# Optimization experiments

Hardware: AMD Instinct MI355X
Metric: run time of the kernel (lower is better)

Reference implementation:

```python
import jax, jax.numpy as jnp
import numpy as np

N = 50000      # nodes
E = 400000     # edges (before self-loops)
F_IN = 128     # input_embedding_dim
HID = 256      # hidden_dim
HEADS = 4      # gat_heads
C1 = HID // HEADS  # per-head channels layer 0
OUT = 128      # output_node_dim
G = 64         # graphs in batch
NEG_SLOPE = 0.2


def setup_inputs() -> dict:
    key = jax.random.key(0)
    ks = jax.random.split(key, 12)
    s = lambda fan: 1.0 / np.sqrt(fan)
    embedded_x = jax.random.normal(ks[0], (N, F_IN), jnp.float32)
    edge_index = jax.random.randint(ks[1], (2, E), 0, N, dtype=jnp.int32)
    batch_idx = jnp.sort(jax.random.randint(ks[2], (N,), 0, G, dtype=jnp.int32))
    # layer 0: GATConv(F_IN -> C1, heads=HEADS, concat=True)
    W1 = jax.random.normal(ks[3], (F_IN, HEADS * C1), jnp.float32) * s(F_IN)
    att_src1 = jax.random.normal(ks[4], (HEADS, C1), jnp.float32) * s(C1)
    att_dst1 = jax.random.normal(ks[5], (HEADS, C1), jnp.float32) * s(C1)
    b1 = jnp.zeros((HEADS * C1,), jnp.float32)
    # layer 1 (last): GATConv(HID -> OUT, heads=1, concat=False)
    W2 = jax.random.normal(ks[6], (HID, OUT), jnp.float32) * s(HID)
    att_src2 = jax.random.normal(ks[7], (1, OUT), jnp.float32) * s(OUT)
    att_dst2 = jax.random.normal(ks[8], (1, OUT), jnp.float32) * s(OUT)
    b2 = jnp.zeros((OUT,), jnp.float32)
    return {"embedded_x": embedded_x, "edge_index": edge_index, "batch_idx": batch_idx,
            "W1": W1, "att_src1": att_src1, "att_dst1": att_dst1, "b1": b1,
            "W2": W2, "att_src2": att_src2, "att_dst2": att_dst2, "b2": b2}


def gat_conv(x, src, dst, W, att_src, att_dst, bias, heads, out_ch, concat):
    n = x.shape[0]
    xw = (x @ W).reshape(n, heads, out_ch)              # [N,H,C]
    a_s = (xw * att_src[None]).sum(-1)                  # [N,H]
    a_d = (xw * att_dst[None]).sum(-1)                  # [N,H]
    e = jax.nn.leaky_relu(a_s[src] + a_d[dst], NEG_SLOPE)  # [E',H]
    # segment softmax over incoming edges of each dst node (self-loops guarantee non-empty)
    m = jax.ops.segment_max(e, dst, num_segments=n)
    ee = jnp.exp(e - m[dst])
    denom = jax.ops.segment_sum(ee, dst, num_segments=n)
    alpha = ee / denom[dst]                             # [E',H]
    msg = xw[src] * alpha[:, :, None]                   # [E',H,C]
    out = jax.ops.segment_sum(msg, dst, num_segments=n) # [N,H,C]
    out = out.reshape(n, heads * out_ch) if concat else out.mean(axis=1)
    return out + bias


def reference(embedded_x, edge_index, batch_idx, W1, att_src1, att_dst1, b1, W2, att_src2, att_dst2, b2):
    loops = jnp.arange(N, dtype=edge_index.dtype)
    src = jnp.concatenate([edge_index[0], loops])
    dst = jnp.concatenate([edge_index[1], loops])
    h = gat_conv(embedded_x, src, dst, W1, att_src1, att_dst1, b1, HEADS, C1, True)
    h = jax.nn.elu(h)  # dropout is identity in eval
    h = gat_conv(h, src, dst, W2, att_src2, att_dst2, b2, 1, OUT, False)
    h = jax.nn.elu(h)
    # final_node_transform is Identity (current_dim == output_node_dim)
    counts = jax.ops.segment_sum(jnp.ones((N,), h.dtype), batch_idx, num_segments=G)
    graph_embedding = jax.ops.segment_sum(h, batch_idx, num_segments=G) / jnp.maximum(counts, 1.0)[:, None]
    return (graph_embedding, h)
```

## Files before the change

### kernel.cpp

```cpp
#include <hip/hip_runtime.h>

#define NN   50000
#define NE   400000
#define NET  450000
#define NG   64
#define NEG  0.2f

using bf16x8 = __attribute__((ext_vector_type(8))) short;
using f32x4  = __attribute__((ext_vector_type(4))) float;

__device__ inline float b2f(unsigned short u){
  union{unsigned int i; float f;} v; v.i = ((unsigned int)u) << 16; return v.f;
}
__device__ inline unsigned short f2b(float f){
  union{float f; unsigned int i;} v; v.f = f;
  unsigned int r = (v.i + 0x7fffu + ((v.i >> 16) & 1u)) >> 16;
  return (unsigned short)r;
}
__device__ inline float sane(float o){
  return (o > -1e30f && o < 1e30f) ? o : 0.f;
}
__device__ inline float lrelu_clamp(float e){
  e = e > 0.f ? e : NEG * e;
  return fminf(e, 60.f);
}

__global__ void pack_w(const float* __restrict__ W, unsigned short* __restrict__ Bp,
                       int K, int N){
  int t = blockIdx.x * blockDim.x + threadIdx.x;
  int nk = K / 32;
  int total = (N / 16) * nk * 64;
  if (t >= total) return;
  int lane = t & 63; int rest = t >> 6;
  int kit = rest % nk; int nt = rest / nk;
  int quad = lane >> 4, n = lane & 15;
  unsigned short* dst = Bp + (size_t)t * 8;
#pragma unroll
  for (int j = 0; j < 8; j++)
    dst[j] = f2b(W[(size_t)(kit*32 + quad*8 + j) * N + nt*16 + n]);
}

__global__ void gemm1_fused(const float* __restrict__ X, const unsigned short* __restrict__ Bp,
                            const float* __restrict__ av, const float* __restrict__ dv,
                            unsigned short* __restrict__ C,
                            float* __restrict__ a_s, float* __restrict__ a_d){
  constexpr int NK = 4, NT = 16;
  int lane = threadIdx.x & 63, wave = threadIdx.x >> 6;
  int mbase = (blockIdx.x * 4 + wave) * 16;
  if (mbase >= NN) return;
  int quad = lane >> 4, nn = lane & 15;
  int arow = mbase + nn; if (arow >= NN) arow = NN - 1;
  const float* Xr = X + (size_t)arow * 128 + quad * 8;
  bf16x8 afrag[NK];
#pragma unroll
  for (int kit = 0; kit < NK; kit++){
    bf16x8 a;
#pragma unroll
    for (int j = 0; j < 8; j++) a[j] = (short)f2b(Xr[kit * 32 + j]);
    afrag[kit] = a;
  }
  float sd0=0,sd1=0,sd2=0,sd3=0, dd0=0,dd1=0,dd2=0,dd3=0;
#pragma unroll
  for (int nt = 0; nt < NT; nt++){
    f32x4 acc = {0.f, 0.f, 0.f, 0.f};
#pragma unroll
    for (int kit = 0; kit < NK; kit++){
      bf16x8 bfrag = *(const bf16x8*)(Bp + ((size_t)(nt*NK + kit) * 64 + lane) * 8);
      acc = __builtin_amdgcn_mfma_f32_16x16x32_bf16(afrag[kit], bfrag, acc, 0, 0, 0);
    }
    int col = nt * 16 + nn;
    float avc = av[col], dvc = dv[col];
    sd0 += acc[0]*avc; dd0 += acc[0]*dvc;
    sd1 += acc[1]*avc; dd1 += acc[1]*dvc;
    sd2 += acc[2]*avc; dd2 += acc[2]*dvc;
    sd3 += acc[3]*avc; dd3 += acc[3]*dvc;
#pragma unroll
    for (int r = 0; r < 4; r++){
      int row = mbase + quad * 4 + r;
      if (row < NN) C[(size_t)row * 256 + col] = f2b(acc[r]);
    }
    if ((nt & 3) == 3){
      int hh = nt >> 2;
#pragma unroll
      for (int off = 1; off < 16; off <<= 1){
        sd0 += __shfl_xor(sd0, off); sd1 += __shfl_xor(sd1, off);
        sd2 += __shfl_xor(sd2, off); sd3 += __shfl_xor(sd3, off);
        dd0 += __shfl_xor(dd0, off); dd1 += __shfl_xor(dd1, off);
        dd2 += __shfl_xor(dd2, off); dd3 += __shfl_xor(dd3, off);
      }
      if (nn == 0){
        int row = mbase + quad * 4;
        if (row + 0 < NN){ a_s[(row+0)*4+hh] = sd0; a_d[(row+0)*4+hh] = dd0; }
        if (row + 1 < NN){ a_s[(row+1)*4+hh] = sd1; a_d[(row+1)*4+hh] = dd1; }
        if (row + 2 < NN){ a_s[(row+2)*4+hh] = sd2; a_d[(row+2)*4+hh] = dd2; }
        if (row + 3 < NN){ a_s[(row+3)*4+hh] = sd3; a_d[(row+3)*4+hh] = dd3; }
      }
      sd0=sd1=sd2=sd3=dd0=dd1=dd2=dd3=0.f;
    }
  }
}

__global__ void gemm2_fused(const unsigned short* __restrict__ A, const unsigned short* __restrict__ Bp,
                            const float* __restrict__ av, const float* __restrict__ dv,
                            unsigned short* __restrict__ C,
                            float* __restrict__ a_s, float* __restrict__ a_d){
  constexpr int NK = 8, NT = 8;
  int lane = threadIdx.x & 63, wave = threadIdx.x >> 6;
  int mbase = (blockIdx.x * 4 + wave) * 16;
  if (mbase >= NN) return;
  int quad = lane >> 4, nn = lane & 15;
  int arow = mbase + nn; if (arow >= NN) arow = NN - 1;
  const unsigned short* Ar = A + (size_t)arow * 256 + quad * 8;
  bf16x8 afrag[NK];
#pragma unroll
  for (int kit = 0; kit < NK; kit++)
    afrag[kit] = *(const bf16x8*)(Ar + kit * 32);
  float sd0=0,sd1=0,sd2=0,sd3=0, dd0=0,dd1=0,dd2=0,dd3=0;
#pragma unroll
  for (int nt = 0; nt < NT; nt++){
    f32x4 acc = {0.f, 0.f, 0.f, 0.f};
#pragma unroll
    for (int kit = 0; kit < NK; kit++){
      bf16x8 bfrag = *(const bf16x8*)(Bp + ((size_t)(nt*NK + kit) * 64 + lane) * 8);
      acc = __builtin_amdgcn_mfma_f32_16x16x32_bf16(afrag[kit], bfrag, acc, 0, 0, 0);
    }
    int col = nt * 16 + nn;
    float avc = av[col], dvc = dv[col];
    sd0 += acc[0]*avc; dd0 += acc[0]*dvc;
    sd1 += acc[1]*avc; dd1 += acc[1]*dvc;
    sd2 += acc[2]*avc; dd2 += acc[2]*dvc;
    sd3 += acc[3]*avc; dd3 += acc[3]*dvc;
#pragma unroll
    for (int r = 0; r < 4; r++){
      int row = mbase + quad * 4 + r;
      if (row < NN) C[(size_t)row * 128 + col] = f2b(acc[r]);
    }
  }
#pragma unroll
  for (int off = 1; off < 16; off <<= 1){
    sd0 += __shfl_xor(sd0, off); sd1 += __shfl_xor(sd1, off);
    sd2 += __shfl_xor(sd2, off); sd3 += __shfl_xor(sd3, off);
    dd0 += __shfl_xor(dd0, off); dd1 += __shfl_xor(dd1, off);
    dd2 += __shfl_xor(dd2, off); dd3 += __shfl_xor(dd3, off);
  }
  if (nn == 0){
    int row = mbase + quad * 4;
    if (row + 0 < NN){ a_s[row+0] = sd0; a_d[row+0] = dd0; }
    if (row + 1 < NN){ a_s[row+1] = sd1; a_d[row+1] = dd1; }
    if (row + 2 < NN){ a_s[row+2] = sd2; a_d[row+2] = dd2; }
    if (row + 3 < NN){ a_s[row+3] = sd3; a_d[row+3] = dd3; }
  }
}

__global__ void count_deg(const int* __restrict__ ei, int* __restrict__ deg){
  int t = blockIdx.x * blockDim.x + threadIdx.x;
  if (t >= NET) return;
  int d = (t < NE) ? ei[NE + t] : (t - NE);
  if (d < 0) d = 0; if (d >= NN) d = NN - 1;
  atomicAdd(&deg[d], 1);
}

__global__ void scan_block(const int* __restrict__ in, int* __restrict__ out_excl,
                           int* __restrict__ bsums, int n){
  __shared__ int s[256];
  int tid = threadIdx.x, gid = blockIdx.x * 256 + tid;
  int v = (gid < n) ? in[gid] : 0;
  s[tid] = v; __syncthreads();
  for (int off = 1; off < 256; off <<= 1){
    int t = (tid >= off) ? s[tid - off] : 0;
    __syncthreads();
    s[tid] += t;
    __syncthreads();
  }
  if (gid < n) out_excl[gid] = s[tid] - v;
  if (tid == 255) bsums[blockIdx.x] = s[255];
}

__global__ void scan_sums(int* __restrict__ bs, int nb){
  __shared__ int s[256];
  int tid = threadIdx.x;
  int v = (tid < nb) ? bs[tid] : 0;
  s[tid] = v; __syncthreads();
  for (int off = 1; off < 256; off <<= 1){
    int t = (tid >= off) ? s[tid - off] : 0;
    __syncthreads();
    s[tid] += t;
    __syncthreads();
  }
  if (tid < nb) bs[tid] = s[tid] - v;
}

__global__ void scan_add(int* __restrict__ offs, const int* __restrict__ bs,
                         int* __restrict__ cursor, int n){
  int gid = blockIdx.x * 256 + threadIdx.x;
  if (gid < n){
    int o = offs[gid] + bs[blockIdx.x];
    offs[gid] = o; cursor[gid] = o;
  }
  if (gid == 0) offs[n] = NET;
}

__global__ void fill_csr(const int* __restrict__ ei, int* __restrict__ cursor,
                         int* __restrict__ csr){
  int t = blockIdx.x * blockDim.x + threadIdx.x;
  if (t >= NET) return;
  int s = (t < NE) ? ei[t]      : (t - NE);
  int d = (t < NE) ? ei[NE + t] : (t - NE);
  if (d < 0) d = 0; if (d >= NN) d = NN - 1;
  int pos = atomicAdd(&cursor[d], 1);
  if (pos >= 0 && pos < NET) csr[pos] = s;
}

__global__ void agg1(const unsigned short* __restrict__ xw, const float* __restrict__ a_s,
                     const float* __restrict__ a_d, const int* __restrict__ offs,
                     const int* __restrict__ csr, const float* __restrict__ bias,
                     unsigned short* __restrict__ h1){
  int lane = threadIdx.x & 63;
  int node = (blockIdx.x * blockDim.x + threadIdx.x) >> 6;
  if (node >= NN) return;
  int h = lane >> 4;
  int beg = offs[node], end = offs[node + 1];
  if (beg < 0) beg = 0; if (end > NET) end = NET;
  float adv = a_d[node * 4 + h];
  float l0=0,l1=0,l2=0,l3=0;
  float c00=0,c01=0,c02=0,c03=0;
  float c10=0,c11=0,c12=0,c13=0;
  float c20=0,c21=0,c22=0,c23=0;
  float c30=0,c31=0,c32=0,c33=0;
  int e = beg;
  for (; e + 4 <= end; e += 4){
    int s0 = csr[e], s1 = csr[e+1], s2 = csr[e+2], s3 = csr[e+3];
    float p0 = __expf(lrelu_clamp(a_s[s0*4+h] + adv));
    float p1 = __expf(lrelu_clamp(a_s[s1*4+h] + adv));
    float p2 = __expf(lrelu_clamp(a_s[s2*4+h] + adv));
    float p3 = __expf(lrelu_clamp(a_s[s3*4+h] + adv));
    ushort4 x0 = *(const ushort4*)(xw + (size_t)s0 * 256 + lane * 4);
    ushort4 x1 = *(const ushort4*)(xw + (size_t)s1 * 256 + lane * 4);
    ushort4 x2 = *(const ushort4*)(xw + (size_t)s2 * 256 + lane * 4);
    ushort4 x3 = *(const ushort4*)(xw + (size_t)s3 * 256 + lane * 4);
    l0 += p0; c00 += p0*b2f(x0.x); c01 += p0*b2f(x0.y); c02 += p0*b2f(x0.z); c03 += p0*b2f(x0.w);
    l1 += p1; c10 += p1*b2f(x1.x); c11 += p1*b2f(x1.y); c12 += p1*b2f(x1.z); c13 += p1*b2f(x1.w);
    l2 += p2; c20 += p2*b2f(x2.x); c21 += p2*b2f(x2.y); c22 += p2*b2f(x2.z); c23 += p2*b2f(x2.w);
    l3 += p3; c30 += p3*b2f(x3.x); c31 += p3*b2f(x3.y); c32 += p3*b2f(x3.z); c33 += p3*b2f(x3.w);
  }
  for (; e < end; e++){
    int s0 = csr[e];
    float p0 = __expf(lrelu_clamp(a_s[s0*4+h] + adv));
    ushort4 x0 = *(const ushort4*)(xw + (size_t)s0 * 256 + lane * 4);
    l0 += p0; c00 += p0*b2f(x0.x); c01 += p0*b2f(x0.y); c02 += p0*b2f(x0.z); c03 += p0*b2f(x0.w);
  }
  float l = l0 + l1 + l2 + l3;
  float C0 = c00 + c10 + c20 + c30;
  float C1 = c01 + c11 + c21 + c31;
  float C2 = c02 + c12 + c22 + c32;
  float C3 = c03 + c13 + c23 + c33;
  if (!(l > 0.f)) l = 1.f;
  float inv = 1.f / l;
  float4 b4 = *(const float4*)(bias + lane * 4);
  float v; ushort4 o;
  v = C0 * inv + b4.x; v = v > 0.f ? v : expm1f(v); o.x = f2b(sane(v));
  v = C1 * inv + b4.y; v = v > 0.f ? v : expm1f(v); o.y = f2b(sane(v));
  v = C2 * inv + b4.z; v = v > 0.f ? v : expm1f(v); o.z = f2b(sane(v));
  v = C3 * inv + b4.w; v = v > 0.f ? v : expm1f(v); o.w = f2b(sane(v));
  *(ushort4*)(h1 + (size_t)node * 256 + lane * 4) = o;
}

__global__ void agg2(const unsigned short* __restrict__ xw, const float* __restrict__ a_s,
                     const float* __restrict__ a_d, const int* __restrict__ offs,
                     const int* __restrict__ csr, const float* __restrict__ bias,
                     float* __restrict__ hout){
  int lane = threadIdx.x & 63;
  int node = (blockIdx.x * blockDim.x + threadIdx.x) >> 6;
  if (node >= NN) return;
  int beg = offs[node], end = offs[node + 1];
  if (beg < 0) beg = 0; if (end > NET) end = NET;
  float adv = a_d[node];
  float l0=0,l1=0,l2=0,l3=0;
  float c00=0,c01=0, c10=0,c11=0, c20=0,c21=0, c30=0,c31=0;
  int e = beg;
  for (; e + 4 <= end; e += 4){
    int s0 = csr[e], s1 = csr[e+1], s2 = csr[e+2], s3 = csr[e+3];
    float p0 = __expf(lrelu_clamp(a_s[s0] + adv));
    float p1 = __expf(lrelu_clamp(a_s[s1] + adv));
    float p2 = __expf(lrelu_clamp(a_s[s2] + adv));
    float p3 = __expf(lrelu_clamp(a_s[s3] + adv));
    ushort2 x0 = *(const ushort2*)(xw + (size_t)s0 * 128 + lane * 2);
    ushort2 x1 = *(const ushort2*)(xw + (size_t)s1 * 128 + lane * 2);
    ushort2 x2 = *(const ushort2*)(xw + (size_t)s2 * 128 + lane * 2);
    ushort2 x3 = *(const ushort2*)(xw + (size_t)s3 * 128 + lane * 2);
    l0 += p0; c00 += p0*b2f(x0.x); c01 += p0*b2f(x0.y);
    l1 += p1; c10 += p1*b2f(x1.x); c11 += p1*b2f(x1.y);
    l2 += p2; c20 += p2*b2f(x2.x); c21 += p2*b2f(x2.y);
    l3 += p3; c30 += p3*b2f(x3.x); c31 += p3*b2f(x3.y);
  }
  for (; e < end; e++){
    int s0 = csr[e];
    float p0 = __expf(lrelu_clamp(a_s[s0] + adv));
    ushort2 x0 = *(const ushort2*)(xw + (size_t)s0 * 128 + lane * 2);
    l0 += p0; c00 += p0*b2f(x0.x); c01 += p0*b2f(x0.y);
  }
  float l = l0 + l1 + l2 + l3;
  float C0 = c00 + c10 + c20 + c30;
  float C1 = c01 + c11 + c21 + c31;
  if (!(l > 0.f)) l = 1.f;
  float inv = 1.f / l;
  float v0 = C0 * inv + bias[lane*2];   v0 = v0 > 0.f ? v0 : expm1f(v0);
  float v1 = C1 * inv + bias[lane*2+1]; v1 = v1 > 0.f ? v1 : expm1f(v1);
  float2 o; o.x = sane(v0); o.y = sane(v1);
  *(float2*)(hout + (size_t)node * 128 + lane * 2) = o;
}

__global__ void pool_kernel(const float* __restrict__ h, const int* __restrict__ batch,
                            float* __restrict__ pools, int* __restrict__ cnt){
  int c = threadIdx.x;
  int n0 = blockIdx.x * 64;
  if (n0 >= NN) return;
  int nend = n0 + 64; if (nend > NN) nend = NN;
  int cur = batch[n0];
  cur = (cur < 0) ? 0 : (cur >= NG ? NG - 1 : cur);
  float sum = 0.f; int count = 0;
  for (int n = n0; n < nend; n++){
    int g = batch[n];
    g = (g < 0) ? 0 : (g >= NG ? NG - 1 : g);
    if (g != cur){
      atomicAdd(&pools[cur * 128 + c], sum);
      if (c == 0) atomicAdd(&cnt[cur], count);
      sum = 0.f; count = 0; cur = g;
    }
    sum += h[(size_t)n * 128 + c];
    count++;
  }
  atomicAdd(&pools[cur * 128 + c], sum);
  if (c == 0) atomicAdd(&cnt[cur], count);
}

__global__ void final_kernel(const float* __restrict__ pools, const int* __restrict__ cnt,
                             float* __restrict__ out){
  int g = blockIdx.x, c = threadIdx.x;
  float d = fmaxf((float)cnt[g], 1.0f);
  out[g * 128 + c] = sane(pools[g * 128 + c] / d);
}

extern "C" void kernel_launch(void* const* d_in, const int* in_sizes, int n_in,
                              void* d_out, int out_size, void* d_ws, size_t ws_size,
                              hipStream_t stream){
  const float* x    = (const float*)d_in[0];
  const int*   ei   = (const int*)d_in[1];
  const int*   bat  = (const int*)d_in[2];
  const float* W1   = (const float*)d_in[3];
  const float* av1  = (const float*)d_in[4];
  const float* dv1  = (const float*)d_in[5];
  const float* b1   = (const float*)d_in[6];
  const float* W2   = (const float*)d_in[7];
  const float* av2  = (const float*)d_in[8];
  const float* dv2  = (const float*)d_in[9];
  const float* b2   = (const float*)d_in[10];

  char* w = (char*)d_ws;
  size_t o = 0;
  auto carve = [&](size_t bytes) -> char* {
    char* p = w + o; o += (bytes + 255) & ~(size_t)255; return p;
  };
  unsigned short* Bp1   = (unsigned short*)carve((size_t)4096 * 8 * 2);
  unsigned short* Bp2   = (unsigned short*)carve((size_t)4096 * 8 * 2);
  float*          a_s1v = (float*)carve((size_t)NN * 4 * 4);
  float*          a_d1v = (float*)carve((size_t)NN * 4 * 4);
  float*          a_s2v = (float*)carve((size_t)NN * 4);
  float*          a_d2v = (float*)carve((size_t)NN * 4);
  int*            deg   = (int*)carve((size_t)NN * 4);
  int*            offs  = (int*)carve((size_t)(NN + 1) * 4);
  int*            cursor= (int*)carve((size_t)NN * 4);
  int*            bsums = (int*)carve(256 * 4);
  int*            csr   = (int*)carve((size_t)NET * 4);
  float*          pools = (float*)carve((size_t)NG * 128 * 4);
  int*            cnt   = (int*)carve((size_t)NG * 4);
  unsigned short* xw1   = (unsigned short*)carve((size_t)NN * 256 * 2);
  unsigned short* h1b   = (unsigned short*)carve((size_t)NN * 256 * 2);
  unsigned short* xw2   = (unsigned short*)carve((size_t)NN * 128 * 2);

  float* out_ge = (float*)d_out;
  float* out_h  = (float*)d_out + NG * 128;

  hipMemsetAsync(deg,   0, (size_t)NN * 4,       stream);
  hipMemsetAsync(pools, 0, (size_t)NG * 128 * 4, stream);
  hipMemsetAsync(cnt,   0, (size_t)NG * 4,       stream);

  pack_w<<<16, 256, 0, stream>>>(W1, Bp1, 128, 256);
  pack_w<<<16, 256, 0, stream>>>(W2, Bp2, 256, 128);

  count_deg<<<(NET + 255) / 256, 256, 0, stream>>>(ei, deg);
  scan_block<<<196, 256, 0, stream>>>(deg, offs, bsums, NN);
  scan_sums<<<1, 256, 0, stream>>>(bsums, 196);
  scan_add<<<196, 256, 0, stream>>>(offs, bsums, cursor, NN);
  fill_csr<<<(NET + 255) / 256, 256, 0, stream>>>(ei, cursor, csr);

  gemm1_fused<<<782, 256, 0, stream>>>(x, Bp1, av1, dv1, xw1, a_s1v, a_d1v);
  agg1<<<12500, 256, 0, stream>>>(xw1, a_s1v, a_d1v, offs, csr, b1, h1b);

  gemm2_fused<<<782, 256, 0, stream>>>(h1b, Bp2, av2, dv2, xw2, a_s2v, a_d2v);
  agg2<<<12500, 256, 0, stream>>>(xw2, a_s2v, a_d2v, offs, csr, b2, out_h);

  pool_kernel<<<782, 128, 0, stream>>>(out_h, bat, pools, cnt);
  final_kernel<<<NG, 128, 0, stream>>>(pools, cnt, out_ge);
}
```

Before: 285.7 us.

## Merge setup launches, unroll aggregation loops to eight edges, shrink pool tiles

Replaces the three memsets with one zeroing kernel and the two weight-pack launches with a single kernel. Folds the block-sum scan into the add pass so each block reduces its own prefix, removing one launch. Unrolls the edge loops in both aggregation kernels to eight edges per step so more gathers are in flight, and gives the pooling kernel 16 nodes per block for more parallelism. The trade-offs are higher register pressure in the aggregation kernels and more atomics in pooling.

```diff
diff --git a/kernel.cpp b/kernel.cpp
--- a/kernel.cpp
+++ b/kernel.cpp
@@ -21,16 +21,19 @@
   return (o > -1e30f && o < 1e30f) ? o : 0.f;
 }
 __device__ inline float lrelu_clamp(float e){
-  e = e > 0.f ? e : NEG * e;
+  e = fmaxf(e, NEG * e);
   return fminf(e, 60.f);
 }
 
-__global__ void pack_w(const float* __restrict__ W, unsigned short* __restrict__ Bp,
-                       int K, int N){
-  int t = blockIdx.x * blockDim.x + threadIdx.x;
+__global__ void zero_all(int* __restrict__ deg, float* __restrict__ pools, int* __restrict__ cnt){
+  int i = blockIdx.x * 256 + threadIdx.x;
+  if (i < NN) deg[i] = 0;
+  if (i < NG * 128) pools[i] = 0.f;
+  if (i < NG) cnt[i] = 0;
+}
+
+__device__ inline void pack_one(const float* W, unsigned short* Bp, int t, int K, int N){
   int nk = K / 32;
-  int total = (N / 16) * nk * 64;
-  if (t >= total) return;
   int lane = t & 63; int rest = t >> 6;
   int kit = rest % nk; int nt = rest / nk;
   int quad = lane >> 4, n = lane & 15;
@@ -38,6 +41,12 @@
 #pragma unroll
   for (int j = 0; j < 8; j++)
     dst[j] = f2b(W[(size_t)(kit*32 + quad*8 + j) * N + nt*16 + n]);
+}
+__global__ void pack_both(const float* __restrict__ W1, const float* __restrict__ W2,
+                          unsigned short* __restrict__ Bp1, unsigned short* __restrict__ Bp2){
+  int t = blockIdx.x * 256 + threadIdx.x;
+  if (t < 4096) pack_one(W1, Bp1, t, 128, 256);
+  else          pack_one(W2, Bp2, t - 4096, 256, 128);
 }
 
 __global__ void gemm1_fused(const float* __restrict__ X, const unsigned short* __restrict__ Bp,
@@ -176,25 +185,21 @@
   if (tid == 255) bsums[blockIdx.x] = s[255];
 }
 
-__global__ void scan_sums(int* __restrict__ bs, int nb){
-  __shared__ int s[256];
-  int tid = threadIdx.x;
-  int v = (tid < nb) ? bs[tid] : 0;
-  s[tid] = v; __syncthreads();
-  for (int off = 1; off < 256; off <<= 1){
-    int t = (tid >= off) ? s[tid - off] : 0;
+__global__ void scan_add2(int* __restrict__ offs, const int* __restrict__ bsums,
+                          int* __restrict__ cursor, int n){
+  __shared__ int lds[256];
+  int b = blockIdx.x, tid = threadIdx.x;
+  int v = 0;
+  for (int i = tid; i < b; i += 256) v += bsums[i];
+  lds[tid] = v; __syncthreads();
+  for (int off = 128; off; off >>= 1){
+    if (tid < off) lds[tid] += lds[tid + off];
     __syncthreads();
-    s[tid] += t;
-    __syncthreads();
-  }
-  if (tid < nb) bs[tid] = s[tid] - v;
-}
-
-__global__ void scan_add(int* __restrict__ offs, const int* __restrict__ bs,
-                         int* __restrict__ cursor, int n){
-  int gid = blockIdx.x * 256 + threadIdx.x;
+  }
+  int prefix = lds[0];
+  int gid = b * 256 + tid;
   if (gid < n){
-    int o = offs[gid] + bs[blockIdx.x];
+    int o = offs[gid] + prefix;
     offs[gid] = o; cursor[gid] = o;
   }
   if (gid == 0) offs[n] = NET;
@@ -228,20 +233,34 @@
   float c20=0,c21=0,c22=0,c23=0;
   float c30=0,c31=0,c32=0,c33=0;
   int e = beg;
-  for (; e + 4 <= end; e += 4){
-    int s0 = csr[e], s1 = csr[e+1], s2 = csr[e+2], s3 = csr[e+3];
+  for (; e + 8 <= end; e += 8){
+    int s0 = csr[e],   s1 = csr[e+1], s2 = csr[e+2], s3 = csr[e+3];
+    int s4 = csr[e+4], s5 = csr[e+5], s6 = csr[e+6], s7 = csr[e+7];
     float p0 = __expf(lrelu_clamp(a_s[s0*4+h] + adv));
     float p1 = __expf(lrelu_clamp(a_s[s1*4+h] + adv));
     float p2 = __expf(lrelu_clamp(a_s[s2*4+h] + adv));
     float p3 = __expf(lrelu_clamp(a_s[s3*4+h] + adv));
+    float p4 = __expf(lrelu_clamp(a_s[s4*4+h] + adv));
+    float p5 = __expf(lrelu_clamp(a_s[s5*4+h] + adv));
+    float p6 = __expf(lrelu_clamp(a_s[s6*4+h] + adv));
+    float p7 = __expf(lrelu_clamp(a_s[s7*4+h] + adv));
     ushort4 x0 = *(const ushort4*)(xw + (size_t)s0 * 256 + lane * 4);
     ushort4 x1 = *(const ushort4*)(xw + (size_t)s1 * 256 + lane * 4);
     ushort4 x2 = *(const ushort4*)(xw + (size_t)s2 * 256 + lane * 4);
     ushort4 x3 = *(const ushort4*)(xw + (size_t)s3 * 256 + lane * 4);
-    l0 += p0; c00 += p0*b2f(x0.x); c01 += p0*b2f(x0.y); c02 += p0*b2f(x0.z); c03 += p0*b2f(x0.w);
-    l1 += p1; c10 += p1*b2f(x1.x); c11 += p1*b2f(x1.y); c12 += p1*b2f(x1.z); c13 += p1*b2f(x1.w);
-    l2 += p2; c20 += p2*b2f(x2.x); c21 += p2*b2f(x2.y); c22 += p2*b2f(x2.z); c23 += p2*b2f(x2.w);
-    l3 += p3; c30 += p3*b2f(x3.x); c31 += p3*b2f(x3.y); c32 += p3*b2f(x3.z); c33 += p3*b2f(x3.w);
+    ushort4 x4 = *(const ushort4*)(xw + (size_t)s4 * 256 + lane * 4);
+    ushort4 x5 = *(const ushort4*)(xw + (size_t)s5 * 256 + lane * 4);
+    ushort4 x6 = *(const ushort4*)(xw + (size_t)s6 * 256 + lane * 4);
+    ushort4 x7 = *(const ushort4*)(xw + (size_t)s7 * 256 + lane * 4);
+    l0 += p0 + p4; l1 += p1 + p5; l2 += p2 + p6; l3 += p3 + p7;
+    c00 += p0*b2f(x0.x); c01 += p0*b2f(x0.y); c02 += p0*b2f(x0.z); c03 += p0*b2f(x0.w);
+    c10 += p1*b2f(x1.x); c11 += p1*b2f(x1.y); c12 += p1*b2f(x1.z); c13 += p1*b2f(x1.w);
+    c20 += p2*b2f(x2.x); c21 += p2*b2f(x2.y); c22 += p2*b2f(x2.z); c23 += p2*b2f(x2.w);
+    c30 += p3*b2f(x3.x); c31 += p3*b2f(x3.y); c32 += p3*b2f(x3.z); c33 += p3*b2f(x3.w);
+    c00 += p4*b2f(x4.x); c01 += p4*b2f(x4.y); c02 += p4*b2f(x4.z); c03 += p4*b2f(x4.w);
+    c10 += p5*b2f(x5.x); c11 += p5*b2f(x5.y); c12 += p5*b2f(x5.z); c13 += p5*b2f(x5.w);
+    c20 += p6*b2f(x6.x); c21 += p6*b2f(x6.y); c22 += p6*b2f(x6.z); c23 += p6*b2f(x6.w);
+    c30 += p7*b2f(x7.x); c31 += p7*b2f(x7.y); c32 += p7*b2f(x7.z); c33 += p7*b2f(x7.w);
   }
   for (; e < end; e++){
     int s0 = csr[e];
@@ -249,11 +268,11 @@
     ushort4 x0 = *(const ushort4*)(xw + (size_t)s0 * 256 + lane * 4);
     l0 += p0; c00 += p0*b2f(x0.x); c01 += p0*b2f(x0.y); c02 += p0*b2f(x0.z); c03 += p0*b2f(x0.w);
   }
-  float l = l0 + l1 + l2 + l3;
-  float C0 = c00 + c10 + c20 + c30;
-  float C1 = c01 + c11 + c21 + c31;
-  float C2 = c02 + c12 + c22 + c32;
-  float C3 = c03 + c13 + c23 + c33;
+  float l = (l0 + l1) + (l2 + l3);
+  float C0 = (c00 + c10) + (c20 + c30);
+  float C1 = (c01 + c11) + (c21 + c31);
+  float C2 = (c02 + c12) + (c22 + c32);
+  float C3 = (c03 + c13) + (c23 + c33);
   if (!(l > 0.f)) l = 1.f;
   float inv = 1.f / l;
   float4 b4 = *(const float4*)(bias + lane * 4);
@@ -278,20 +297,34 @@
   float l0=0,l1=0,l2=0,l3=0;
   float c00=0,c01=0, c10=0,c11=0, c20=0,c21=0, c30=0,c31=0;
   int e = beg;
-  for (; e + 4 <= end; e += 4){
-    int s0 = csr[e], s1 = csr[e+1], s2 = csr[e+2], s3 = csr[e+3];
+  for (; e + 8 <= end; e += 8){
+    int s0 = csr[e],   s1 = csr[e+1], s2 = csr[e+2], s3 = csr[e+3];
+    int s4 = csr[e+4], s5 = csr[e+5], s6 = csr[e+6], s7 = csr[e+7];
     float p0 = __expf(lrelu_clamp(a_s[s0] + adv));
     float p1 = __expf(lrelu_clamp(a_s[s1] + adv));
     float p2 = __expf(lrelu_clamp(a_s[s2] + adv));
     float p3 = __expf(lrelu_clamp(a_s[s3] + adv));
+    float p4 = __expf(lrelu_clamp(a_s[s4] + adv));
+    float p5 = __expf(lrelu_clamp(a_s[s5] + adv));
+    float p6 = __expf(lrelu_clamp(a_s[s6] + adv));
+    float p7 = __expf(lrelu_clamp(a_s[s7] + adv));
     ushort2 x0 = *(const ushort2*)(xw + (size_t)s0 * 128 + lane * 2);
     ushort2 x1 = *(const ushort2*)(xw + (size_t)s1 * 128 + lane * 2);
     ushort2 x2 = *(const ushort2*)(xw + (size_t)s2 * 128 + lane * 2);
     ushort2 x3 = *(const ushort2*)(xw + (size_t)s3 * 128 + lane * 2);
-    l0 += p0; c00 += p0*b2f(x0.x); c01 += p0*b2f(x0.y);
-    l1 += p1; c10 += p1*b2f(x1.x); c11 += p1*b2f(x1.y);
-    l2 += p2; c20 += p2*b2f(x2.x); c21 += p2*b2f(x2.y);
-    l3 += p3; c30 += p3*b2f(x3.x); c31 += p3*b2f(x3.y);
+    ushort2 x4 = *(const ushort2*)(xw + (size_t)s4 * 128 + lane * 2);
+    ushort2 x5 = *(const ushort2*)(xw + (size_t)s5 * 128 + lane * 2);
+    ushort2 x6 = *(const ushort2*)(xw + (size_t)s6 * 128 + lane * 2);
+    ushort2 x7 = *(const ushort2*)(xw + (size_t)s7 * 128 + lane * 2);
+    l0 += p0 + p4; l1 += p1 + p5; l2 += p2 + p6; l3 += p3 + p7;
+    c00 += p0*b2f(x0.x); c01 += p0*b2f(x0.y);
+    c10 += p1*b2f(x1.x); c11 += p1*b2f(x1.y);
+    c20 += p2*b2f(x2.x); c21 += p2*b2f(x2.y);
+    c30 += p3*b2f(x3.x); c31 += p3*b2f(x3.y);
+    c00 += p4*b2f(x4.x); c01 += p4*b2f(x4.y);
+    c10 += p5*b2f(x5.x); c11 += p5*b2f(x5.y);
+    c20 += p6*b2f(x6.x); c21 += p6*b2f(x6.y);
+    c30 += p7*b2f(x7.x); c31 += p7*b2f(x7.y);
   }
   for (; e < end; e++){
     int s0 = csr[e];
@@ -299,9 +332,9 @@
     ushort2 x0 = *(const ushort2*)(xw + (size_t)s0 * 128 + lane * 2);
     l0 += p0; c00 += p0*b2f(x0.x); c01 += p0*b2f(x0.y);
   }
-  float l = l0 + l1 + l2 + l3;
-  float C0 = c00 + c10 + c20 + c30;
-  float C1 = c01 + c11 + c21 + c31;
+  float l = (l0 + l1) + (l2 + l3);
+  float C0 = (c00 + c10) + (c20 + c30);
+  float C1 = (c01 + c11) + (c21 + c31);
   if (!(l > 0.f)) l = 1.f;
   float inv = 1.f / l;
   float v0 = C0 * inv + bias[lane*2];   v0 = v0 > 0.f ? v0 : expm1f(v0);
@@ -313,9 +346,9 @@
 __global__ void pool_kernel(const float* __restrict__ h, const int* __restrict__ batch,
                             float* __restrict__ pools, int* __restrict__ cnt){
   int c = threadIdx.x;
-  int n0 = blockIdx.x * 64;
+  int n0 = blockIdx.x * 16;
   if (n0 >= NN) return;
-  int nend = n0 + 64; if (nend > NN) nend = NN;
+  int nend = n0 + 16; if (nend > NN) nend = NN;
   int cur = batch[n0];
   cur = (cur < 0) ? 0 : (cur >= NG ? NG - 1 : cur);
   float sum = 0.f; int count = 0;
@@ -381,17 +414,12 @@
   float* out_ge = (float*)d_out;
   float* out_h  = (float*)d_out + NG * 128;
 
-  hipMemsetAsync(deg,   0, (size_t)NN * 4,       stream);
-  hipMemsetAsync(pools, 0, (size_t)NG * 128 * 4, stream);
-  hipMemsetAsync(cnt,   0, (size_t)NG * 4,       stream);
-
-  pack_w<<<16, 256, 0, stream>>>(W1, Bp1, 128, 256);
-  pack_w<<<16, 256, 0, stream>>>(W2, Bp2, 256, 128);
+  zero_all<<<196, 256, 0, stream>>>(deg, pools, cnt);
+  pack_both<<<32, 256, 0, stream>>>(W1, W2, Bp1, Bp2);
 
   count_deg<<<(NET + 255) / 256, 256, 0, stream>>>(ei, deg);
   scan_block<<<196, 256, 0, stream>>>(deg, offs, bsums, NN);
-  scan_sums<<<1, 256, 0, stream>>>(bsums, 196);
-  scan_add<<<196, 256, 0, stream>>>(offs, bsums, cursor, NN);
+  scan_add2<<<196, 256, 0, stream>>>(offs, bsums, cursor, NN);
   fill_csr<<<(NET + 255) / 256, 256, 0, stream>>>(ei, cursor, csr);
 
   gemm1_fused<<<782, 256, 0, stream>>>(x, Bp1, av1, dv1, xw1, a_s1v, a_d1v);
@@ -400,6 +428,6 @@
   gemm2_fused<<<782, 256, 0, stream>>>(h1b, Bp2, av2, dv2, xw2, a_s2v, a_d2v);
   agg2<<<12500, 256, 0, stream>>>(xw2, a_s2v, a_d2v, offs, csr, b2, out_h);
 
-  pool_kernel<<<782, 128, 0, stream>>>(out_h, bat, pools, cnt);
+  pool_kernel<<<3125, 128, 0, stream>>>(out_h, bat, pools, cnt);
   final_kernel<<<NG, 128, 0, stream>>>(pools, cnt, out_ge);
 }
```

New measurement: 286.2 us. Within noise of the previous version (+0.2%).
